# Kernel tuning notes

Measured on AMD Instinct MI355X. Metric: run time of the kernel, lower is better.

Reference implementation:

```python
import jax, jax.numpy as jnp
import numpy as np

N = 4096      # nodes
IN = 512      # input_size
D = 128       # output_size per head
H = 4         # num_heads
SLOPE = 0.2   # leaky relu negative slope
NEG = -1e30   # masked-out logit value (finite to keep softmax grad-safe)


def setup_inputs() -> dict:
    key = jax.random.key(0)
    ks = jax.random.split(key, 8)
    stdv = 1.0 / np.sqrt(H * D)
    inputs = jax.random.normal(ks[0], (N, IN), jnp.float32)
    adjacency = jax.random.randint(ks[1], (N, N), 0, 2).astype(jnp.float32)  # dense 0/1 mask
    weight = jax.random.uniform(ks[2], (IN, H * D), jnp.float32, -stdv, stdv)
    weight_u = jax.random.uniform(ks[3], (H, D, 1), jnp.float32, -1.0, 1.0)
    weight_v = jax.random.uniform(ks[4], (H, D, 1), jnp.float32, -1.0, 1.0)
    bias = jax.random.uniform(ks[5], (1, H * D), jnp.float32, -stdv, stdv)
    proj_w = jax.random.normal(ks[6], (IN, H * D), jnp.float32) * 0.02
    proj_b = jnp.zeros((H * D,), jnp.float32)
    return {"inputs": inputs, "adjacency": adjacency, "weight": weight,
            "weight_u": weight_u, "weight_v": weight_v, "bias": bias,
            "proj_w": proj_w, "proj_b": proj_b}


def reference(inputs, adjacency, weight, weight_u, weight_v, bias, proj_w, proj_b):
    # support: [H, N, D]
    support = (inputs @ weight).reshape(N, H, D).transpose(1, 0, 2)
    # f1: per-source scores [H, 1, N]; f2: per-dest scores [H, N, 1]
    f1 = jnp.einsum('hnd,hdo->hn', support, weight_u)[:, None, :]
    f2 = jnp.einsum('hnd,hdo->hn', support, weight_v)[:, :, None]
    logits = f1 + f2                                  # [H, N, N]
    w = jnp.where(logits >= 0, logits, SLOPE * logits)  # leaky_relu
    masked = w * adjacency[None]                      # [H, N, N]
    # torch to_sparse keeps nonzero entries; sparse softmax treats the rest as -inf
    mask = masked != 0
    z = jnp.where(mask, masked, NEG)
    attn = jax.nn.softmax(z, axis=-1) * mask          # rows with no edges -> all zeros
    out = jnp.einsum('hij,hjd->hid', attn, support)   # [H, N, D]
    out = out.transpose(1, 0, 2).reshape(N, H * D)
    out = out + bias
    out = out + inputs @ proj_w + proj_b              # residual projection
    return out
```

## Files before the change

kernel.cpp:

```cpp
#include <hip/hip_runtime.h>

#define NN 4096
#define IND 512
#define HD 512
#define NH 4
#define DH 128
#define K3 1536

typedef __attribute__((ext_vector_type(8))) short bf16x8;
typedef __attribute__((ext_vector_type(4))) float f32x4;
typedef __attribute__((ext_vector_type(4))) unsigned short us4;
typedef __attribute__((ext_vector_type(8))) unsigned short us8;

typedef __attribute__((address_space(3))) void lds_void;
typedef const __attribute__((address_space(1))) void glob_void;

__device__ __forceinline__ void gll16(const void* g, void* l) {
  __builtin_amdgcn_global_load_lds((glob_void*)g, (lds_void*)l, 16, 0, 0);
}

__device__ __forceinline__ unsigned short f2bf(float x) {
  union { float f; unsigned u; } a; a.f = x;
  unsigned r = a.u + 0x7FFFu + ((a.u >> 16) & 1u);
  return (unsigned short)(r >> 16);
}
__device__ __forceinline__ float bf2f(unsigned short b) {
  union { float f; unsigned u; } a; a.u = ((unsigned)b) << 16;
  return a.f;
}

__global__ __launch_bounds__(256) void prep_inputs(const float* __restrict__ x,
                                                   unsigned short* __restrict__ A3) {
  int idx = blockIdx.x * 256 + threadIdx.x;
  int n = idx >> 7, c4 = (idx & 127) * 4;
  f32x4 v = *(const f32x4*)(x + (size_t)n * IND + c4);
  us4 hi, lo;
#pragma unroll
  for (int e = 0; e < 4; ++e) {
    hi[e] = f2bf(v[e]);
    lo[e] = f2bf(v[e] - bf2f(hi[e]));
  }
  size_t base = (size_t)n * K3 + c4;
  *(us4*)(A3 + base) = hi;
  *(us4*)(A3 + base + 512) = hi;
  *(us4*)(A3 + base + 1024) = lo;
}

__global__ __launch_bounds__(256) void prep_weights(const float* __restrict__ w,
                                                    const float* __restrict__ pw,
                                                    unsigned short* __restrict__ B3T,
                                                    unsigned short* __restrict__ PhT) {
  int idx = blockIdx.x * 256 + threadIdx.x;
  int c = idx >> 9, k = idx & 511;
  float v = w[(size_t)k * HD + c];
  unsigned short hi = f2bf(v);
  unsigned short lo = f2bf(v - bf2f(hi));
  size_t base = (size_t)c * K3;
  B3T[base + k] = hi;
  B3T[base + 512 + k] = lo;
  B3T[base + 1024 + k] = hi;
  float p = pw[(size_t)k * HD + c];
  PhT[(size_t)c * IND + k] = f2bf(p);
}

__global__ __launch_bounds__(256) void gemm_kernel(
    const unsigned short* __restrict__ A3, const unsigned short* __restrict__ B3T,
    const unsigned short* __restrict__ PhT,
    unsigned short* __restrict__ ST, float* __restrict__ resid,
    float* __restrict__ g1, float* __restrict__ g2,
    const float* __restrict__ wu, const float* __restrict__ wv,
    const float* __restrict__ projb, const float* __restrict__ bias) {
  const int z = blockIdx.z;
  int L = blockIdx.x + 32 * blockIdx.y;
  int xcd = L & 7, idx = L >> 3;
  const int by = idx & 3;
  const int bx = (idx >> 2) * 8 + xcd;
  const unsigned short* Bp = z ? PhT : B3T;
  const int ldb = z ? IND : K3;
  const int K = z ? IND : K3;
  const int m0 = bx * 128;
  const int n0 = by * 128;
  const int tid = threadIdx.x;
  const int lane = tid & 63;
  const int wvv_ = tid >> 6;
  const int wm = wvv_ & 1, wn = wvv_ >> 1;
  const int lrow = lane & 15;
  const int kg = lane >> 4;

  __shared__ __align__(16) unsigned short sh[32768];

  f32x4 acc[4][4];
#pragma unroll
  for (int a = 0; a < 4; ++a)
#pragma unroll
    for (int b = 0; b < 4; ++b) acc[a][b] = (f32x4){0.f, 0.f, 0.f, 0.f};

  auto STAGE = [&](int buf, int k0) {
    unsigned short* Asb = sh + buf * 8192;
    unsigned short* Bsb = sh + 16384 + buf * 8192;
#pragma unroll
    for (int s = 0; s < 4; ++s) {
      int c = s * 256 + tid;
      int rr = c >> 3, sl = c & 7;
      int ko = sl ^ (rr & 7);
      gll16(A3 + (size_t)(m0 + rr) * K3 + k0 + ko * 8, Asb + c * 8);
    }
#pragma unroll
    for (int s = 0; s < 4; ++s) {
      int c = s * 256 + tid;
      int rr = c >> 3, sl = c & 7;
      int ko = sl ^ (rr & 7);
      gll16(Bp + (size_t)(n0 + rr) * ldb + k0 + ko * 8, Bsb + c * 8);
    }
  };

  STAGE(0, 0);
  __syncthreads();

  int buf = 0;
  for (int k0 = 0; k0 < K; k0 += 64) {
    if (k0 + 64 < K) STAGE(buf ^ 1, k0 + 64);
    const unsigned short* Asb = sh + buf * 8192;
    const unsigned short* Bsb = sh + 16384 + buf * 8192;
#pragma unroll
    for (int ks = 0; ks < 2; ++ks) {
      int cb = ks * 4 + kg;
      bf16x8 af[4], bfr[4];
#pragma unroll
      for (int mf = 0; mf < 4; ++mf) {
        int row = wm * 64 + mf * 16 + lrow;
        af[mf] = *(const bf16x8*)(Asb + row * 64 + (cb ^ (row & 7)) * 8);
      }
#pragma unroll
      for (int nf = 0; nf < 4; ++nf) {
        int row = wn * 64 + nf * 16 + lrow;
        bfr[nf] = *(const bf16x8*)(Bsb + row * 64 + (cb ^ (row & 7)) * 8);
      }
#pragma unroll
      for (int mf = 0; mf < 4; ++mf)
#pragma unroll
        for (int nf = 0; nf < 4; ++nf)
          acc[mf][nf] = __builtin_amdgcn_mfma_f32_16x16x32_bf16(af[mf], bfr[nf], acc[mf][nf], 0, 0, 0);
    }
    __syncthreads();
    buf ^= 1;
  }

  const int lcol = lane & 15;
  if (z == 0) {
    float wuv[4], wvvv[4];
#pragma unroll
    for (int nf = 0; nf < 4; ++nf) {
      int cg = n0 + wn * 64 + nf * 16 + lcol;
      wuv[nf] = wu[cg]; wvvv[nf] = wv[cg];
    }
    float du[4][4], dv[4][4];
#pragma unroll
    for (int mf = 0; mf < 4; ++mf)
#pragma unroll
      for (int q = 0; q < 4; ++q) {
        float a = 0.f, b = 0.f;
#pragma unroll
        for (int nf = 0; nf < 4; ++nf) {
          a += acc[mf][nf][q] * wuv[nf];
          b += acc[mf][nf][q] * wvvv[nf];
        }
#pragma unroll
        for (int m = 1; m < 16; m <<= 1) {
          a += __shfl_xor(a, m);
          b += __shfl_xor(b, m);
        }
        du[mf][q] = a; dv[mf][q] = b;
      }
    float* f12 = (float*)(sh + 17920);
    if (lcol == 0) {
#pragma unroll
      for (int mf = 0; mf < 4; ++mf)
#pragma unroll
        for (int q = 0; q < 4; ++q) {
          int rowl = wm * 64 + mf * 16 + kg * 4 + q;
          f12[wn * 128 + rowl] = du[mf][q];
          f12[256 + wn * 128 + rowl] = dv[mf][q];
        }
    }
    unsigned short* lst = sh;
#pragma unroll
    for (int mf = 0; mf < 4; ++mf)
#pragma unroll
      for (int nf = 0; nf < 4; ++nf) {
        int coll = wn * 64 + nf * 16 + lcol;
        int row4 = wm * 64 + mf * 16 + kg * 4;
        us4 st4;
#pragma unroll
        for (int q = 0; q < 4; ++q) st4[q] = f2bf(acc[mf][nf][q]);
        *(us4*)(&lst[coll * 136 + row4]) = st4;
      }
    __syncthreads();
    {
      int row = tid & 127, sel = tid >> 7;
      float vs = f12[sel * 256 + row] + f12[sel * 256 + 128 + row];
      float* gp = sel ? g2 : g1;
      gp[by * NN + m0 + row] = vs * 1.4426950408889634f;
    }
#pragma unroll
    for (int k = 0; k < 8; ++k) {
      int col = k * 16 + (tid >> 4);
      int chunk = tid & 15;
      us8 v = *(const us8*)(&lst[col * 136 + chunk * 8]);
      *(us8*)(ST + (size_t)(n0 + col) * NN + m0 + chunk * 8) = v;
    }
  } else {
#pragma unroll
    for (int mf = 0; mf < 4; ++mf)
#pragma unroll
      for (int nf = 0; nf < 4; ++nf) {
        int rg = m0 + wm * 64 + mf * 16 + kg * 4;
        int cg = n0 + wn * 64 + nf * 16 + lcol;
        float addv = projb[cg] + bias[cg];
#pragma unroll
        for (int q = 0; q < 4; ++q)
          resid[(size_t)(rg + q) * HD + cg] = acc[mf][nf][q] + addv;
      }
  }
}

__global__ __launch_bounds__(256) void ballot_kernel(const float* __restrict__ adj,
                                                     unsigned long long* __restrict__ bmT) {
  int i = blockIdx.x;
  int tid = threadIdx.x, lane = tid & 63, wvv_ = tid >> 6;
  const float* arow = adj + (size_t)i * NN;
#pragma unroll 4
  for (int it = 0; it < 16; ++it) {
    int j = it * 256 + tid;
    unsigned long long b = __ballot(arow[j] != 0.0f);
    if (lane == 0) bmT[(size_t)(it * 4 + wvv_) * NN + i] = b;
  }
}

__global__ __launch_bounds__(256, 2) void attn_kernel(
    const unsigned short* __restrict__ ST,
    const unsigned long long* __restrict__ bmT,
    const float* __restrict__ g1, const float* __restrict__ g2,
    const float* __restrict__ resid, float* __restrict__ out) {
  const int bx = blockIdx.x;
  const int by = blockIdx.y;
  const int tid = threadIdx.x;
  const int lane = tid & 63;
  const int w = tid >> 6;
  const int il = lane & 15;
  const int kg = lane >> 4;
  const int i0 = bx * 32;

  __shared__ unsigned short tile[4][2][4096];

  const float g2v0 = g2[by * NN + i0 + il];
  const float g2v1 = g2[by * NN + i0 + il + 16];
  const float g2v0h = 0.2f * g2v0, g2v1h = 0.2f * g2v1;
  const float* g1h = g1 + by * NN + w * 1024;
  const unsigned short* STh = ST + (size_t)(by * 128) * NN + w * 1024;
  const unsigned char* mb0 = (const unsigned char*)bmT + ((size_t)(i0 + il) << 3) + kg;
  const unsigned char* mb1 = mb0 + 128;

  const int dr0 = lane >> 2;
  const int jq = (lane & 3) ^ ((lane >> 3) & 3);
  const unsigned short* src0 = STh + (size_t)dr0 * NN + jq * 8;

  auto STAGE = [&](int buf, int J) {
#pragma unroll
    for (int s = 0; s < 8; ++s)
      gll16(src0 + (size_t)s * 16 * NN + J, &tile[w][buf][s * 512]);
  };
  auto MOFF = [&](int t) -> size_t {
    return ((size_t)(w * 16 + (t >> 1)) * (NN * 8)) + (size_t)((t & 1) * 4);
  };

  const int rb = il * 32 + (kg ^ ((il >> 1) & 3)) * 8;

  bf16x8 ones;
#pragma unroll
  for (int e = 0; e < 8; ++e) ones[e] = (short)0x3F80;

  f32x4 acc[2][8];
#pragma unroll
  for (int g = 0; g < 2; ++g)
#pragma unroll
    for (int d = 0; d < 8; ++d) acc[g][d] = (f32x4){0.f, 0.f, 0.f, 0.f};
  f32x4 asum0 = (f32x4){0.f, 0.f, 0.f, 0.f};
  f32x4 asum1 = (f32x4){0.f, 0.f, 0.f, 0.f};

  STAGE(0, 0);
  f32x4 g1c0 = *(const f32x4*)(g1h + kg * 8);
  f32x4 g1c1 = *(const f32x4*)(g1h + kg * 8 + 4);
  unsigned mbc0 = mb0[MOFF(0)];
  unsigned mbc1 = mb1[MOFF(0)];
  f32x4 g1n0, g1n1;
  unsigned mbn0 = 0, mbn1 = 0;

  int buf = 0;
  for (int t = 0; t < 32; ++t) {
    if (t < 31) {
      STAGE(buf ^ 1, (t + 1) * 32);
      int tn = t + 1;
      g1n0 = *(const f32x4*)(g1h + tn * 32 + kg * 8);
      g1n1 = *(const f32x4*)(g1h + tn * 32 + kg * 8 + 4);
      size_t mo = MOFF(tn);
      mbn0 = mb0[mo];
      mbn1 = mb1[mo];
      asm volatile("s_waitcnt vmcnt(12)" ::: "memory");
    } else {
      asm volatile("s_waitcnt vmcnt(0)" ::: "memory");
    }
    const unsigned short* tb = &tile[w][buf][0];
    bf16x8 bc[8];
#pragma unroll
    for (int d = 0; d < 8; ++d)
      bc[d] = *(const bf16x8*)(tb + d * 512 + rb);

    union F8 { f32x4 v[2]; float f[8]; } gc;
    gc.v[0] = g1c0; gc.v[1] = g1c1;
    float p0[8], p1[8];
#pragma unroll
    for (int e = 0; e < 8; ++e) {
      float t0 = gc.f[e] + g2v0;
      float b0 = __builtin_fmaf(0.2f, gc.f[e], g2v0h);
      float pe0 = __builtin_amdgcn_exp2f(fmaxf(t0, b0));
      union { float f; unsigned u; } u0; u0.f = pe0;
      u0.u &= (unsigned)(-(int)((mbc0 >> e) & 1u));
      p0[e] = u0.f;
      float t1 = gc.f[e] + g2v1;
      float b1 = __builtin_fmaf(0.2f, gc.f[e], g2v1h);
      float pe1 = __builtin_amdgcn_exp2f(fmaxf(t1, b1));
      union { float f; unsigned u; } u1; u1.f = pe1;
      u1.u &= (unsigned)(-(int)((mbc1 >> e) & 1u));
      p1[e] = u1.f;
    }
    union { unsigned u[4]; bf16x8 v; } af0, af1;
#pragma unroll
    for (int e2 = 0; e2 < 4; ++e2) {
      unsigned pk;
      asm("v_cvt_pk_bf16_f32 %0, %1, %2" : "=v"(pk) : "v"(p0[2 * e2]), "v"(p0[2 * e2 + 1]));
      af0.u[e2] = pk;
      asm("v_cvt_pk_bf16_f32 %0, %1, %2" : "=v"(pk) : "v"(p1[2 * e2]), "v"(p1[2 * e2 + 1]));
      af1.u[e2] = pk;
    }
    __builtin_amdgcn_s_setprio(1);
#pragma unroll
    for (int d = 0; d < 8; ++d) {
      acc[0][d] = __builtin_amdgcn_mfma_f32_16x16x32_bf16(af0.v, bc[d], acc[0][d], 0, 0, 0);
      acc[1][d] = __builtin_amdgcn_mfma_f32_16x16x32_bf16(af1.v, bc[d], acc[1][d], 0, 0, 0);
    }
    asum0 = __builtin_amdgcn_mfma_f32_16x16x32_bf16(af0.v, ones, asum0, 0, 0, 0);
    asum1 = __builtin_amdgcn_mfma_f32_16x16x32_bf16(af1.v, ones, asum1, 0, 0, 0);
    __builtin_amdgcn_s_setprio(0);

    g1c0 = g1n0; g1c1 = g1n1; mbc0 = mbn0; mbc1 = mbn1;
    buf ^= 1;
  }

  __syncthreads();
  float* fl = (float*)&tile[0][0][0];
  if (il == 0) {
#pragma unroll
    for (int q = 0; q < 4; ++q) {
      fl[w * 4096 + kg * 4 + q] = asum0[q];
      fl[w * 4096 + 16 + kg * 4 + q] = asum1[q];
    }
  }
  __syncthreads();
  const int row = tid >> 3, cb = tid & 7;
  float ssum = fl[row] + fl[4096 + row] + fl[8192 + row] + fl[12288 + row];
  float rs = ssum > 0.0f ? 1.0f / ssum : 0.0f;
  __syncthreads();
#pragma unroll
  for (int g = 0; g < 2; ++g)
#pragma unroll
    for (int d = 0; d < 8; ++d)
#pragma unroll
      for (int q = 0; q < 4; ++q)
        fl[w * 4096 + (g * 16 + kg * 4 + q) * 128 + d * 16 + il] =
            (g ? acc[1][d][q] : acc[0][d][q]);
  __syncthreads();
  const float* rres = resid + (size_t)(i0 + row) * HD + by * 128 + cb * 16;
  float* po = out + (size_t)(i0 + row) * HD + by * 128 + cb * 16;
#pragma unroll
  for (int q4 = 0; q4 < 4; ++q4) {
    int o = row * 128 + cb * 16 + q4 * 4;
    f32x4 s0 = *(const f32x4*)(&fl[o]);
    f32x4 s1 = *(const f32x4*)(&fl[4096 + o]);
    f32x4 s2 = *(const f32x4*)(&fl[8192 + o]);
    f32x4 s3 = *(const f32x4*)(&fl[12288 + o]);
    f32x4 rr = *(const f32x4*)(rres + q4 * 4);
    f32x4 ov;
#pragma unroll
    for (int q = 0; q < 4; ++q)
      ov[q] = (s0[q] + s1[q] + s2[q] + s3[q]) * rs + rr[q];
    *(f32x4*)(po + q4 * 4) = ov;
  }
}

extern "C" void kernel_launch(void* const* d_in, const int* in_sizes, int n_in,
                              void* d_out, int out_size, void* d_ws, size_t ws_size,
                              hipStream_t stream) {
  const float* inputs = (const float*)d_in[0];
  const float* adj = (const float*)d_in[1];
  const float* weight = (const float*)d_in[2];
  const float* wu = (const float*)d_in[3];
  const float* wv = (const float*)d_in[4];
  const float* bias = (const float*)d_in[5];
  const float* projw = (const float*)d_in[6];
  const float* projb = (const float*)d_in[7];
  float* out = (float*)d_out;

  char* ws = (char*)d_ws;
  size_t off = 0;
  unsigned short* A3 = (unsigned short*)(ws + off); off += (size_t)NN * K3 * 2;
  unsigned short* B3T = (unsigned short*)(ws + off); off += (size_t)HD * K3 * 2;
  unsigned short* PhT = (unsigned short*)(ws + off); off += (size_t)HD * IND * 2;
  unsigned short* ST = (unsigned short*)(ws + off); off += (size_t)HD * NN * 2;
  float* resid = (float*)(ws + off); off += (size_t)NN * HD * 4;
  float* g1 = (float*)(ws + off); off += (size_t)NH * NN * 4;
  float* g2 = (float*)(ws + off); off += (size_t)NH * NN * 4;
  unsigned long long* bmT = (unsigned long long*)(ws + off); off += (size_t)NN * 64 * 8;

  prep_inputs<<<(NN * IND) / 1024, 256, 0, stream>>>(inputs, A3);
  prep_weights<<<(IND * HD) / 256, 256, 0, stream>>>(weight, projw, B3T, PhT);
  gemm_kernel<<<dim3(32, 4, 2), 256, 0, stream>>>(A3, B3T, PhT, ST, resid, g1, g2,
                                                  wu, wv, projb, bias);
  ballot_kernel<<<NN, 256, 0, stream>>>(adj, bmT);
  attn_kernel<<<dim3(128, 4), 256, 0, stream>>>(ST, bmT, g1, g2, resid, out);
}
```

Before: 198.7 us.

## Split attention over source halves with 64-row tiles and add merge kernel

The attention kernel now handles 64 destination rows per block instead of 32, and splits the source dimension into two halves across blockIdx.z. Each staged support tile is therefore reused by four MFMA row groups, which halves tile loads per output. Partial numerators and row sums go to workspace buffers that reuse the dead A3 region, and a new merge kernel combines them, normalizes, and adds the residual. The two prep kernels are fused into one launch, and the leaky-relu logit is simplified to fmaxf(a, 0.2a). The cost is extra global traffic for the partial results plus one more launch, and higher register pressure from 128 accumulator floats per thread.

After: 197.1 us. Within noise of the previous version (-0.8%).

```diff
diff --git a/kernel.cpp b/kernel.cpp
--- a/kernel.cpp
+++ b/kernel.cpp
@@ -29,38 +29,39 @@
   return a.f;
 }
 
-__global__ __launch_bounds__(256) void prep_inputs(const float* __restrict__ x,
-                                                   unsigned short* __restrict__ A3) {
-  int idx = blockIdx.x * 256 + threadIdx.x;
-  int n = idx >> 7, c4 = (idx & 127) * 4;
-  f32x4 v = *(const f32x4*)(x + (size_t)n * IND + c4);
-  us4 hi, lo;
-#pragma unroll
-  for (int e = 0; e < 4; ++e) {
-    hi[e] = f2bf(v[e]);
-    lo[e] = f2bf(v[e] - bf2f(hi[e]));
-  }
-  size_t base = (size_t)n * K3 + c4;
-  *(us4*)(A3 + base) = hi;
-  *(us4*)(A3 + base + 512) = hi;
-  *(us4*)(A3 + base + 1024) = lo;
-}
-
-__global__ __launch_bounds__(256) void prep_weights(const float* __restrict__ w,
-                                                    const float* __restrict__ pw,
-                                                    unsigned short* __restrict__ B3T,
-                                                    unsigned short* __restrict__ PhT) {
-  int idx = blockIdx.x * 256 + threadIdx.x;
-  int c = idx >> 9, k = idx & 511;
-  float v = w[(size_t)k * HD + c];
-  unsigned short hi = f2bf(v);
-  unsigned short lo = f2bf(v - bf2f(hi));
-  size_t base = (size_t)c * K3;
-  B3T[base + k] = hi;
-  B3T[base + 512 + k] = lo;
-  B3T[base + 1024 + k] = hi;
-  float p = pw[(size_t)k * HD + c];
-  PhT[(size_t)c * IND + k] = f2bf(p);
+__global__ __launch_bounds__(256) void prep_kernel(
+    const float* __restrict__ x, const float* __restrict__ w,
+    const float* __restrict__ pw,
+    unsigned short* __restrict__ A3, unsigned short* __restrict__ B3T,
+    unsigned short* __restrict__ PhT) {
+  int bid = blockIdx.x;
+  if (bid < 2048) {
+    int idx = bid * 256 + threadIdx.x;
+    int n = idx >> 7, c4 = (idx & 127) * 4;
+    f32x4 v = *(const f32x4*)(x + (size_t)n * IND + c4);
+    us4 hi, lo;
+#pragma unroll
+    for (int e = 0; e < 4; ++e) {
+      hi[e] = f2bf(v[e]);
+      lo[e] = f2bf(v[e] - bf2f(hi[e]));
+    }
+    size_t base = (size_t)n * K3 + c4;
+    *(us4*)(A3 + base) = hi;
+    *(us4*)(A3 + base + 512) = hi;
+    *(us4*)(A3 + base + 1024) = lo;
+  } else {
+    int idx = (bid - 2048) * 256 + threadIdx.x;
+    int c = idx >> 9, k = idx & 511;
+    float v = w[(size_t)k * HD + c];
+    unsigned short hi = f2bf(v);
+    unsigned short lo = f2bf(v - bf2f(hi));
+    size_t base = (size_t)c * K3;
+    B3T[base + k] = hi;
+    B3T[base + 512 + k] = lo;
+    B3T[base + 1024 + k] = hi;
+    float p = pw[(size_t)k * HD + c];
+    PhT[(size_t)c * IND + k] = f2bf(p);
+  }
 }
 
 __global__ __launch_bounds__(256) void gemm_kernel(
@@ -241,38 +242,38 @@
     const unsigned short* __restrict__ ST,
     const unsigned long long* __restrict__ bmT,
     const float* __restrict__ g1, const float* __restrict__ g2,
-    const float* __restrict__ resid, float* __restrict__ out) {
+    float* __restrict__ P0, float* __restrict__ P1, float* __restrict__ S) {
   const int bx = blockIdx.x;
   const int by = blockIdx.y;
+  const int bz = blockIdx.z;
   const int tid = threadIdx.x;
   const int lane = tid & 63;
   const int w = tid >> 6;
   const int il = lane & 15;
   const int kg = lane >> 4;
-  const int i0 = bx * 32;
+  const int i0 = bx * 64;
 
   __shared__ unsigned short tile[4][2][4096];
 
-  const float g2v0 = g2[by * NN + i0 + il];
-  const float g2v1 = g2[by * NN + i0 + il + 16];
-  const float g2v0h = 0.2f * g2v0, g2v1h = 0.2f * g2v1;
-  const float* g1h = g1 + by * NN + w * 1024;
-  const unsigned short* STh = ST + (size_t)(by * 128) * NN + w * 1024;
-  const unsigned char* mb0 = (const unsigned char*)bmT + ((size_t)(i0 + il) << 3) + kg;
-  const unsigned char* mb1 = mb0 + 128;
+  float g2v[4];
+#pragma unroll
+  for (int g = 0; g < 4; ++g) g2v[g] = g2[by * NN + i0 + g * 16 + il];
+
+  const float* g1h = g1 + by * NN + bz * 2048 + w * 512;
+  const unsigned short* STh = ST + (size_t)(by * 128) * NN + bz * 2048 + w * 512;
+  const unsigned char* mbp0 = (const unsigned char*)bmT + ((size_t)(i0 + il) << 3) + kg;
+  auto MOFF = [&](int t) -> size_t {
+    return ((size_t)(bz * 32 + w * 8 + (t >> 1)) * (NN * 8)) + (size_t)((t & 1) * 4);
+  };
 
   const int dr0 = lane >> 2;
   const int jq = (lane & 3) ^ ((lane >> 3) & 3);
   const unsigned short* src0 = STh + (size_t)dr0 * NN + jq * 8;
-
   auto STAGE = [&](int buf, int J) {
 #pragma unroll
     for (int s = 0; s < 8; ++s)
       gll16(src0 + (size_t)s * 16 * NN + J, &tile[w][buf][s * 512]);
   };
-  auto MOFF = [&](int t) -> size_t {
-    return ((size_t)(w * 16 + (t >> 1)) * (NN * 8)) + (size_t)((t & 1) * 4);
-  };
 
   const int rb = il * 32 + (kg ^ ((il >> 1) & 3)) * 8;
 
@@ -280,33 +281,36 @@
 #pragma unroll
   for (int e = 0; e < 8; ++e) ones[e] = (short)0x3F80;
 
-  f32x4 acc[2][8];
-#pragma unroll
-  for (int g = 0; g < 2; ++g)
+  f32x4 acc[4][8];
+#pragma unroll
+  for (int g = 0; g < 4; ++g)
 #pragma unroll
     for (int d = 0; d < 8; ++d) acc[g][d] = (f32x4){0.f, 0.f, 0.f, 0.f};
-  f32x4 asum0 = (f32x4){0.f, 0.f, 0.f, 0.f};
-  f32x4 asum1 = (f32x4){0.f, 0.f, 0.f, 0.f};
+  f32x4 asum[4];
+#pragma unroll
+  for (int g = 0; g < 4; ++g) asum[g] = (f32x4){0.f, 0.f, 0.f, 0.f};
 
   STAGE(0, 0);
   f32x4 g1c0 = *(const f32x4*)(g1h + kg * 8);
   f32x4 g1c1 = *(const f32x4*)(g1h + kg * 8 + 4);
-  unsigned mbc0 = mb0[MOFF(0)];
-  unsigned mbc1 = mb1[MOFF(0)];
+  unsigned mbc[4], mbn[4] = {0, 0, 0, 0};
+  {
+    size_t mo = MOFF(0);
+#pragma unroll
+    for (int g = 0; g < 4; ++g) mbc[g] = mbp0[mo + g * 128];
+  }
   f32x4 g1n0, g1n1;
-  unsigned mbn0 = 0, mbn1 = 0;
 
   int buf = 0;
-  for (int t = 0; t < 32; ++t) {
-    if (t < 31) {
+  for (int t = 0; t < 16; ++t) {
+    if (t < 15) {
       STAGE(buf ^ 1, (t + 1) * 32);
-      int tn = t + 1;
-      g1n0 = *(const f32x4*)(g1h + tn * 32 + kg * 8);
-      g1n1 = *(const f32x4*)(g1h + tn * 32 + kg * 8 + 4);
-      size_t mo = MOFF(tn);
-      mbn0 = mb0[mo];
-      mbn1 = mb1[mo];
-      asm volatile("s_waitcnt vmcnt(12)" ::: "memory");
+      g1n0 = *(const f32x4*)(g1h + (t + 1) * 32 + kg * 8);
+      g1n1 = *(const f32x4*)(g1h + (t + 1) * 32 + kg * 8 + 4);
+      size_t mo = MOFF(t + 1);
+#pragma unroll
+      for (int g = 0; g < 4; ++g) mbn[g] = mbp0[mo + g * 128];
+      asm volatile("s_waitcnt vmcnt(14)" ::: "memory");
     } else {
       asm volatile("s_waitcnt vmcnt(0)" ::: "memory");
     }
@@ -318,42 +322,35 @@
 
     union F8 { f32x4 v[2]; float f[8]; } gc;
     gc.v[0] = g1c0; gc.v[1] = g1c1;
-    float p0[8], p1[8];
-#pragma unroll
-    for (int e = 0; e < 8; ++e) {
-      float t0 = gc.f[e] + g2v0;
-      float b0 = __builtin_fmaf(0.2f, gc.f[e], g2v0h);
-      float pe0 = __builtin_amdgcn_exp2f(fmaxf(t0, b0));
-      union { float f; unsigned u; } u0; u0.f = pe0;
-      u0.u &= (unsigned)(-(int)((mbc0 >> e) & 1u));
-      p0[e] = u0.f;
-      float t1 = gc.f[e] + g2v1;
-      float b1 = __builtin_fmaf(0.2f, gc.f[e], g2v1h);
-      float pe1 = __builtin_amdgcn_exp2f(fmaxf(t1, b1));
-      union { float f; unsigned u; } u1; u1.f = pe1;
-      u1.u &= (unsigned)(-(int)((mbc1 >> e) & 1u));
-      p1[e] = u1.f;
-    }
-    union { unsigned u[4]; bf16x8 v; } af0, af1;
-#pragma unroll
-    for (int e2 = 0; e2 < 4; ++e2) {
-      unsigned pk;
-      asm("v_cvt_pk_bf16_f32 %0, %1, %2" : "=v"(pk) : "v"(p0[2 * e2]), "v"(p0[2 * e2 + 1]));
-      af0.u[e2] = pk;
-      asm("v_cvt_pk_bf16_f32 %0, %1, %2" : "=v"(pk) : "v"(p1[2 * e2]), "v"(p1[2 * e2 + 1]));
-      af1.u[e2] = pk;
-    }
-    __builtin_amdgcn_s_setprio(1);
-#pragma unroll
-    for (int d = 0; d < 8; ++d) {
-      acc[0][d] = __builtin_amdgcn_mfma_f32_16x16x32_bf16(af0.v, bc[d], acc[0][d], 0, 0, 0);
-      acc[1][d] = __builtin_amdgcn_mfma_f32_16x16x32_bf16(af1.v, bc[d], acc[1][d], 0, 0, 0);
-    }
-    asum0 = __builtin_amdgcn_mfma_f32_16x16x32_bf16(af0.v, ones, asum0, 0, 0, 0);
-    asum1 = __builtin_amdgcn_mfma_f32_16x16x32_bf16(af1.v, ones, asum1, 0, 0, 0);
-    __builtin_amdgcn_s_setprio(0);
-
-    g1c0 = g1n0; g1c1 = g1n1; mbc0 = mbn0; mbc1 = mbn1;
+#pragma unroll
+    for (int g = 0; g < 4; ++g) {
+      float p[8];
+#pragma unroll
+      for (int e = 0; e < 8; ++e) {
+        float a = gc.f[e] + g2v[g];
+        float m = fmaxf(a, 0.2f * a);
+        float pe = __builtin_amdgcn_exp2f(m);
+        union { float f; unsigned u; } pu; pu.f = pe;
+        pu.u &= (unsigned)(-(int)((mbc[g] >> e) & 1u));
+        p[e] = pu.f;
+      }
+      union { unsigned u[4]; bf16x8 v; } af;
+#pragma unroll
+      for (int e2 = 0; e2 < 4; ++e2) {
+        unsigned pk;
+        asm("v_cvt_pk_bf16_f32 %0, %1, %2" : "=v"(pk) : "v"(p[2 * e2]), "v"(p[2 * e2 + 1]));
+        af.u[e2] = pk;
+      }
+      __builtin_amdgcn_s_setprio(1);
+#pragma unroll
+      for (int d = 0; d < 8; ++d)
+        acc[g][d] = __builtin_amdgcn_mfma_f32_16x16x32_bf16(af.v, bc[d], acc[g][d], 0, 0, 0);
+      asum[g] = __builtin_amdgcn_mfma_f32_16x16x32_bf16(af.v, ones, asum[g], 0, 0, 0);
+      __builtin_amdgcn_s_setprio(0);
+    }
+    g1c0 = g1n0; g1c1 = g1n1;
+#pragma unroll
+    for (int g = 0; g < 4; ++g) mbc[g] = mbn[g];
     buf ^= 1;
   }
 
@@ -361,41 +358,69 @@
   float* fl = (float*)&tile[0][0][0];
   if (il == 0) {
 #pragma unroll
-    for (int q = 0; q < 4; ++q) {
-      fl[w * 4096 + kg * 4 + q] = asum0[q];
-      fl[w * 4096 + 16 + kg * 4 + q] = asum1[q];
-    }
+    for (int g = 0; g < 4; ++g)
+#pragma unroll
+      for (int q = 0; q < 4; ++q)
+        fl[w * 64 + g * 16 + kg * 4 + q] = asum[g][q];
   }
   __syncthreads();
-  const int row = tid >> 3, cb = tid & 7;
-  float ssum = fl[row] + fl[4096 + row] + fl[8192 + row] + fl[12288 + row];
-  float rs = ssum > 0.0f ? 1.0f / ssum : 0.0f;
+  if (tid < 64) {
+    float s = fl[tid] + fl[64 + tid] + fl[128 + tid] + fl[192 + tid];
+    S[((size_t)bz * 4 + by) * NN + i0 + tid] = s;
+  }
   __syncthreads();
-#pragma unroll
-  for (int g = 0; g < 2; ++g)
-#pragma unroll
-    for (int d = 0; d < 8; ++d)
-#pragma unroll
-      for (int q = 0; q < 4; ++q)
-        fl[w * 4096 + (g * 16 + kg * 4 + q) * 128 + d * 16 + il] =
-            (g ? acc[1][d][q] : acc[0][d][q]);
-  __syncthreads();
-  const float* rres = resid + (size_t)(i0 + row) * HD + by * 128 + cb * 16;
-  float* po = out + (size_t)(i0 + row) * HD + by * 128 + cb * 16;
-#pragma unroll
-  for (int q4 = 0; q4 < 4; ++q4) {
-    int o = row * 128 + cb * 16 + q4 * 4;
-    f32x4 s0 = *(const f32x4*)(&fl[o]);
-    f32x4 s1 = *(const f32x4*)(&fl[4096 + o]);
-    f32x4 s2 = *(const f32x4*)(&fl[8192 + o]);
-    f32x4 s3 = *(const f32x4*)(&fl[12288 + o]);
-    f32x4 rr = *(const f32x4*)(rres + q4 * 4);
-    f32x4 ov;
-#pragma unroll
-    for (int q = 0; q < 4; ++q)
-      ov[q] = (s0[q] + s1[q] + s2[q] + s3[q]) * rs + rr[q];
-    *(f32x4*)(po + q4 * 4) = ov;
-  }
+  float* P = bz ? P1 : P0;
+#pragma unroll
+  for (int pass = 0; pass < 2; ++pass) {
+#pragma unroll
+    for (int gg = 0; gg < 2; ++gg) {
+      int g = pass * 2 + gg;
+#pragma unroll
+      for (int d = 0; d < 8; ++d)
+#pragma unroll
+        for (int q = 0; q < 4; ++q)
+          fl[w * 4096 + (gg * 16 + kg * 4 + q) * 128 + d * 16 + il] =
+              acc[g][d][q];
+    }
+    __syncthreads();
+    {
+      int r = tid >> 3, cb = tid & 7;
+      float* prow = P + (size_t)(i0 + pass * 32 + r) * HD + by * 128 + cb * 16;
+#pragma unroll
+      for (int q4 = 0; q4 < 4; ++q4) {
+        int o = r * 128 + cb * 16 + q4 * 4;
+        f32x4 s0 = *(const f32x4*)(&fl[o]);
+        f32x4 s1 = *(const f32x4*)(&fl[4096 + o]);
+        f32x4 s2 = *(const f32x4*)(&fl[8192 + o]);
+        f32x4 s3 = *(const f32x4*)(&fl[12288 + o]);
+        f32x4 ov;
+#pragma unroll
+        for (int q = 0; q < 4; ++q) ov[q] = s0[q] + s1[q] + s2[q] + s3[q];
+        *(f32x4*)(prow + q4 * 4) = ov;
+      }
+    }
+    __syncthreads();
+  }
+}
+
+__global__ __launch_bounds__(256) void merge_kernel(const float* __restrict__ P0,
+                                                    const float* __restrict__ P1,
+                                                    const float* __restrict__ S,
+                                                    const float* __restrict__ resid,
+                                                    float* __restrict__ out) {
+  int idx = blockIdx.x * 256 + threadIdx.x;
+  int i = idx >> 7;
+  int c = (idx & 127) * 4;
+  int h = c >> 7;
+  f32x4 v0 = *(const f32x4*)(P0 + (size_t)i * HD + c);
+  f32x4 v1 = *(const f32x4*)(P1 + (size_t)i * HD + c);
+  float s = S[(size_t)h * NN + i] + S[(size_t)(4 + h) * NN + i];
+  float rs = s > 0.0f ? 1.0f / s : 0.0f;
+  f32x4 rr = *(const f32x4*)(resid + (size_t)i * HD + c);
+  f32x4 o;
+#pragma unroll
+  for (int q = 0; q < 4; ++q) o[q] = (v0[q] + v1[q]) * rs + rr[q];
+  *(f32x4*)(out + (size_t)i * HD + c) = o;
 }
 
 extern "C" void kernel_launch(void* const* d_in, const int* in_sizes, int n_in,
@@ -422,10 +447,14 @@
   float* g2 = (float*)(ws + off); off += (size_t)NH * NN * 4;
   unsigned long long* bmT = (unsigned long long*)(ws + off); off += (size_t)NN * 64 * 8;
 
-  prep_inputs<<<(NN * IND) / 1024, 256, 0, stream>>>(inputs, A3);
-  prep_weights<<<(IND * HD) / 256, 256, 0, stream>>>(weight, projw, B3T, PhT);
+  float* P0 = (float*)(ws + 0);
+  float* S = (float*)(ws + (size_t)NN * HD * 4);
+  float* P1 = (float*)(ws + off); off += (size_t)NN * HD * 4;
+
+  prep_kernel<<<3072, 256, 0, stream>>>(inputs, weight, projw, A3, B3T, PhT);
   gemm_kernel<<<dim3(32, 4, 2), 256, 0, stream>>>(A3, B3T, PhT, ST, resid, g1, g2,
                                                   wu, wv, projb, bias);
   ballot_kernel<<<NN, 256, 0, stream>>>(adj, bmT);
-  attn_kernel<<<dim3(128, 4), 256, 0, stream>>>(ST, bmT, g1, g2, resid, out);
-}
+  attn_kernel<<<dim3(64, 4, 2), 256, 0, stream>>>(ST, bmT, g1, g2, P0, P1, S);
+  merge_kernel<<<2048, 256, 0, stream>>>(P0, P1, S, resid, out);
+}
```
